# Performance work log

Measured on AMD Instinct MI355X. Metric: run time of the kernel, lower is better.

Reference implementation:

```python
import jax, jax.numpy as jnp
import numpy as np

N, E, D_IN, D_HID, D_OUT, G = 50000, 800000, 64, 64, 64, 64
BN_EPS = 1e-5


def gcn_conv(x, W, b, src, dst, n_nodes):
    """PyG GCNConv: add self-loops, sym-normalized sum aggregation, then bias.
    out_i = sum_{j->i} d_j^-1/2 d_i^-1/2 (x W)_j + d_i^-1 (x W)_i + b
    where d_i = 1 + in-degree(i) (self-loop included)."""
    h = x @ W  # [N, out]
    deg = jax.ops.segment_sum(jnp.ones((src.shape[0],), h.dtype), dst,
                              num_segments=n_nodes) + 1.0  # self-loop
    dinv = jax.lax.rsqrt(deg)  # deg >= 1 always
    coef = dinv[src] * dinv[dst]  # [E]
    msgs = h[src] * coef[:, None]  # [E, out] -- the big gather
    agg = jax.ops.segment_sum(msgs, dst, num_segments=n_nodes)
    agg = agg + h * (dinv * dinv)[:, None]  # self-loop messages
    return agg + b


def global_mean_pool(x, batch, n_graphs):
    sums = jax.ops.segment_sum(x, batch, num_segments=n_graphs)
    cnts = jax.ops.segment_sum(jnp.ones((x.shape[0],), x.dtype), batch,
                               num_segments=n_graphs)
    return sums / jnp.maximum(cnts, 1.0)[:, None]


def setup_inputs() -> dict:
    key = jax.random.key(0)
    ks = jax.random.split(key, 8)
    x = jax.random.normal(ks[0], (N, D_IN), dtype=jnp.float32)
    edge_index = jax.random.randint(ks[1], (2, E), 0, N, dtype=jnp.int32)
    batch = jnp.sort(jax.random.randint(ks[2], (N,), 0, G, dtype=jnp.int32))
    s1 = 1.0 / np.sqrt(D_IN)
    s2 = 1.0 / np.sqrt(D_HID)
    W1 = jax.random.uniform(ks[3], (D_IN, D_HID), jnp.float32, -s1, s1)
    b1 = jnp.zeros((D_HID,), jnp.float32)
    gamma = jnp.ones((D_HID,), jnp.float32)
    beta = jnp.zeros((D_HID,), jnp.float32)
    W2 = jax.random.uniform(ks[4], (D_HID, D_OUT), jnp.float32, -s2, s2)
    b2 = jnp.zeros((D_OUT,), jnp.float32)
    return {"x": x, "edge_index": edge_index, "batch": batch,
            "W1": W1, "b1": b1, "gamma": gamma, "beta": beta,
            "W2": W2, "b2": b2}


def reference(x, edge_index, batch, W1, b1, gamma, beta, W2, b2):
    src, dst = edge_index[0], edge_index[1]
    h = gcn_conv(x, W1, b1, src, dst, N)
    # BatchNorm1d with batch statistics (training-mode forward)
    mu = jnp.mean(h, axis=0)
    var = jnp.mean(jnp.square(h - mu), axis=0)
    h = (h - mu) * jax.lax.rsqrt(var + BN_EPS) * gamma + beta
    h = jax.nn.elu(h)
    # dropout is identity in eval / deterministic reference
    out = gcn_conv(h, W2, b2, src, dst, N)
    graph_rep = global_mean_pool(out, batch, G)
    return (out, graph_rep)
```

## Files before the change

kernel.cpp:

```cpp
#include <hip/hip_runtime.h>


constexpr int GGRAPHS = 64;
constexpr int EPB = 4096;
constexpr int CNTB = 128;
constexpr int ZBLK = 32;

__global__ void fat_phist_cnt_zero_mm64_kernel(
    const int* __restrict__ dst, const int* __restrict__ batch,
    int* __restrict__ hist, int* __restrict__ cntR, float* __restrict__ zbase,
    const float* __restrict__ X, const float* __restrict__ W,
    float* __restrict__ Y,
    int E, int n, int nblk, int nbuck) {
  __shared__ float Ws[64][64];
  __shared__ float xs[4][64];
  __shared__ int h[256];
  __shared__ int hb[GGRAPHS];
  int t = threadIdx.x;
  int bid = blockIdx.x;
  if (bid < nblk) {
    h[t] = 0;
    __syncthreads();
    int e0 = bid * EPB;
    int e1 = e0 + EPB < E ? e0 + EPB : E;
    for (int i = e0 + t; i < e1; i += 256) {
      int d = dst[i];
      if ((unsigned)d < (unsigned)n) atomicAdd(&h[d >> 8], 1);
    }
    __syncthreads();
    if (t < nbuck) hist[t * nblk + bid] = h[t];
  } else if (bid < nblk + CNTB) {
    int cb = bid - nblk;
    if (t < GGRAPHS) hb[t] = 0;
    __syncthreads();
    for (int i = cb * 256 + t; i < n; i += CNTB * 256) {
      int g = batch[i];
      if ((unsigned)g < (unsigned)GGRAPHS) atomicAdd(&hb[g], 1);
    }
    __syncthreads();
    if (t < GGRAPHS) cntR[cb * 64 + t] = hb[t];
  } else if (bid < nblk + CNTB + ZBLK) {
    int zb = bid - nblk - CNTB;
    float4 z4 = make_float4(0.f, 0.f, 0.f, 0.f);
    int tot4 = (256 * 128 + 16 * 4096) >> 2;
    float4* d4 = (float4*)zbase;
    for (int i = zb * 256 + t; i < tot4; i += ZBLK * 256) d4[i] = z4;
  } else {
    int mb = bid - nblk - CNTB - ZBLK;
    for (int i = t; i < 64 * 64; i += 256) Ws[i >> 6][i & 63] = W[i];
    int rr = t >> 6, c = t & 63;
    int row = mb * 4 + rr;
    xs[rr][c] = (row < n) ? X[(size_t)row * 64 + c] : 0.0f;
    __syncthreads();
    float acc = 0.0f;
#pragma unroll
    for (int k = 0; k < 64; ++k) acc = fmaf(xs[rr][k], Ws[k][c], acc);
    if (row < n) Y[(size_t)row * 64 + c] = acc;
  }
}

__global__ void scan1_kernel(const int* __restrict__ in, int* __restrict__ out,
                             int* __restrict__ bsum, int n) {
  __shared__ int tmp[256];
  int t = threadIdx.x;
  int i = blockIdx.x * 256 + t;
  int v = (i < n) ? in[i] : 0;
  tmp[t] = v;
  __syncthreads();
#pragma unroll
  for (int off = 1; off < 256; off <<= 1) {
    int a = (t >= off) ? tmp[t - off] : 0;
    __syncthreads();
    tmp[t] += a;
    __syncthreads();
  }
  if (i < n) out[i] = tmp[t] - v;
  if (t == 255) bsum[blockIdx.x] = tmp[255];
}

__global__ void part_kernel(const int* __restrict__ srcp, const int* __restrict__ dstp,
                            const int* __restrict__ hist, const int* __restrict__ bsum,
                            int* __restrict__ part, int E, int n, int nblk, int nbuck,
                            int nbt) {
  __shared__ int tmp[256];
  __shared__ int cur[256];
  int t = threadIdx.x;
  int v = (t < nbt) ? bsum[t] : 0;
  tmp[t] = v;
  __syncthreads();
#pragma unroll
  for (int off = 1; off < 256; off <<= 1) {
    int a = (t >= off) ? tmp[t - off] : 0;
    __syncthreads();
    tmp[t] += a;
    __syncthreads();
  }
  if (t < nbuck) {
    int idx = t * nblk + blockIdx.x;
    int tile = idx >> 8;
    int pre = (tile == 0) ? 0 : tmp[tile - 1];
    cur[t] = hist[idx] + pre;
  }
  __syncthreads();
  int e0 = blockIdx.x * EPB;
  int e1 = e0 + EPB < E ? e0 + EPB : E;
  for (int i = e0 + t; i < e1; i += 256) {
    int d = dstp[i];
    if ((unsigned)d >= (unsigned)n) continue;
    int s = srcp[i];
    int pos = atomicAdd(&cur[d >> 8], 1);
    part[pos] = (s << 8) | (d & 255);
  }
}

__global__ void csr_kernel(const int* __restrict__ part, const int* __restrict__ hist,
                           const int* __restrict__ bsum,
                           int* __restrict__ rowptr, float* __restrict__ dinv,
                           int* __restrict__ col, int n, int nblk, int nbuck,
                           int nbt, int S) {
  __shared__ int tmpb[256];
  __shared__ int degL[256], scn[256], cur[256];
  int t = threadIdx.x;
  int b = blockIdx.x;
  int v = (t < nbt) ? bsum[t] : 0;
  tmpb[t] = v;
  degL[t] = 0;
  cur[t] = 0;
  __syncthreads();
#pragma unroll
  for (int off = 1; off < 256; off <<= 1) {
    int a = (t >= off) ? tmpb[t - off] : 0;
    __syncthreads();
    tmpb[t] += a;
    __syncthreads();
  }
  int bidx = b * nblk;
  int eidx = bidx + nblk;
  int base = hist[bidx] + ((bidx >> 8) ? tmpb[(bidx >> 8) - 1] : 0);
  int total = tmpb[nbt - 1];
  int end = (eidx < S) ? hist[eidx] + ((eidx >> 8) ? tmpb[(eidx >> 8) - 1] : 0) : total;
  for (int i = base + t; i < end; i += 256) atomicAdd(&degL[part[i] & 255], 1);
  __syncthreads();
  int dv = degL[t];
  scn[t] = dv;
  __syncthreads();
#pragma unroll
  for (int off = 1; off < 256; off <<= 1) {
    int a = (t >= off) ? scn[t - off] : 0;
    __syncthreads();
    scn[t] += a;
    __syncthreads();
  }
  int excl = scn[t] - dv;
  int node = (b << 8) + t;
  if (node < n) {
    rowptr[node] = base + excl;
    dinv[node] = rsqrtf((float)dv + 1.0f);
  }
  if (b == nbuck - 1 && t == 0) rowptr[n] = end;
  scn[t] = excl;
  __syncthreads();
  for (int i = base + t; i < end; i += 256) {
    int u = part[i];
    int d = u & 255;
    int k = atomicAdd(&cur[d], 1);
    col[base + scn[d] + k] = u >> 8;
  }
}

__global__ void bn_elu_mm64_kernel(const float* __restrict__ X, const float* __restrict__ W,
                                   const float* __restrict__ ss, float* __restrict__ Y, int n) {
  __shared__ float Ws[64][64];
  __shared__ float xs[4][64];
  int tid = threadIdx.x;
  for (int i = tid; i < 64 * 64; i += 256) Ws[i >> 6][i & 63] = W[i];
  int rr = tid >> 6, c = tid & 63;
  int row = blockIdx.x * 4 + rr;
  float v = 0.0f;
  if (row < n) {
    v = X[(size_t)row * 64 + c] * ss[c] + ss[64 + c];
    v = v > 0.0f ? v : expm1f(v);
  }
  xs[rr][c] = v;
  __syncthreads();
  float acc = 0.0f;
#pragma unroll
  for (int k = 0; k < 64; ++k) acc = fmaf(xs[rr][k], Ws[k][c], acc);
  if (row < n) Y[(size_t)row * 64 + c] = acc;
}

__device__ __forceinline__ float4 gcn_gather_core(
    const int* __restrict__ rowptr, const int* __restrict__ col,
    const float* __restrict__ dinv, const float4* __restrict__ H4,
    int row, int lane, int sub, int cg, bool valid) {
  float4 acc = make_float4(0.f, 0.f, 0.f, 0.f);
  int p0 = 0, p1 = 0;
  if (valid) { p0 = rowptr[row]; p1 = rowptr[row + 1]; }
  for (int base = p0; base < p1; base += 64) {
    int myp = base + lane;
    int j = (myp < p1) ? col[myp] : 0;
    float w = (myp < p1) ? dinv[j] : 0.0f;
    int m = p1 - base;
    m = m < 64 ? m : 64;
#pragma unroll 4
    for (int k = 0; k < m; k += 4) {
      int s = k + sub;
      int jj = __shfl(j, s);
      float ww = __shfl(w, s);
      float4 hv = H4[(size_t)jj * 16 + cg];
      acc.x = fmaf(hv.x, ww, acc.x);
      acc.y = fmaf(hv.y, ww, acc.y);
      acc.z = fmaf(hv.z, ww, acc.z);
      acc.w = fmaf(hv.w, ww, acc.w);
    }
  }
  acc.x += __shfl_xor(acc.x, 16);
  acc.y += __shfl_xor(acc.y, 16);
  acc.z += __shfl_xor(acc.z, 16);
  acc.w += __shfl_xor(acc.w, 16);
  acc.x += __shfl_xor(acc.x, 32);
  acc.y += __shfl_xor(acc.y, 32);
  acc.z += __shfl_xor(acc.z, 32);
  acc.w += __shfl_xor(acc.w, 32);
  return acc;
}

__global__ void gather_bn_kernel(const int* __restrict__ rowptr, const int* __restrict__ col,
                                 const float* __restrict__ dinv, const float* __restrict__ H,
                                 const float* __restrict__ b, float* __restrict__ OUT,
                                 float* __restrict__ bnsR, int n) {
  int wave = threadIdx.x >> 6;
  int lane = threadIdx.x & 63;
  int row = blockIdx.x * 4 + wave;
  bool valid = row < n;
  int sub = lane >> 4;
  int cg = lane & 15;
  const float4* __restrict__ H4 = (const float4*)H;
  float4 acc = gcn_gather_core(rowptr, col, dinv, H4, row, lane, sub, cg, valid);
  float4 o = make_float4(0.f, 0.f, 0.f, 0.f);
  if (valid) {
    float di = dinv[row];
    float d2 = di * di;
    float4 self = H4[(size_t)row * 16 + cg];
    float4 bb = ((const float4*)b)[cg];
    o.x = fmaf(acc.x, di, fmaf(self.x, d2, bb.x));
    o.y = fmaf(acc.y, di, fmaf(self.y, d2, bb.y));
    o.z = fmaf(acc.z, di, fmaf(self.z, d2, bb.z));
    o.w = fmaf(acc.w, di, fmaf(self.w, d2, bb.w));
    if (sub == 0) ((float4*)OUT)[(size_t)row * 16 + cg] = o;
  }
  __shared__ float sA[4][64], sB[4][64];
  if (sub == 0) {
    sA[wave][4 * cg + 0] = o.x;
    sA[wave][4 * cg + 1] = o.y;
    sA[wave][4 * cg + 2] = o.z;
    sA[wave][4 * cg + 3] = o.w;
    sB[wave][4 * cg + 0] = o.x * o.x;
    sB[wave][4 * cg + 1] = o.y * o.y;
    sB[wave][4 * cg + 2] = o.z * o.z;
    sB[wave][4 * cg + 3] = o.w * o.w;
  }
  __syncthreads();
  int t = threadIdx.x;
  if (t < 64) {
    float s = sA[0][t] + sA[1][t] + sA[2][t] + sA[3][t];
    float s2 = sB[0][t] + sB[1][t] + sB[2][t] + sB[3][t];
    float* d = bnsR + (size_t)(blockIdx.x & 255) * 128;
    atomicAdd(&d[t], s);
    atomicAdd(&d[64 + t], s2);
  }
}

__global__ void gather_pool_kernel(const int* __restrict__ rowptr, const int* __restrict__ col,
                                   const float* __restrict__ dinv, const float* __restrict__ H,
                                   const float* __restrict__ b, float* __restrict__ OUT,
                                   const int* __restrict__ batch, float* __restrict__ poolR,
                                   int n) {
  int wave = threadIdx.x >> 6;
  int lane = threadIdx.x & 63;
  int row = blockIdx.x * 4 + wave;
  bool valid = row < n;
  int sub = lane >> 4;
  int cg = lane & 15;
  const float4* __restrict__ H4 = (const float4*)H;
  float4 acc = gcn_gather_core(rowptr, col, dinv, H4, row, lane, sub, cg, valid);
  float4 o = make_float4(0.f, 0.f, 0.f, 0.f);
  __shared__ float sO[4][64];
  __shared__ int sG[4];
  if (valid) {
    float di = dinv[row];
    float d2 = di * di;
    float4 self = H4[(size_t)row * 16 + cg];
    float4 bb = ((const float4*)b)[cg];
    o.x = fmaf(acc.x, di, fmaf(self.x, d2, bb.x));
    o.y = fmaf(acc.y, di, fmaf(self.y, d2, bb.y));
    o.z = fmaf(acc.z, di, fmaf(self.z, d2, bb.z));
    o.w = fmaf(acc.w, di, fmaf(self.w, d2, bb.w));
    if (sub == 0) ((float4*)OUT)[(size_t)row * 16 + cg] = o;
  }
  if (lane == 0) {
    int g = valid ? batch[row] : -1;
    sG[wave] = ((unsigned)g < (unsigned)GGRAPHS) ? g : -1;
  }
  if (sub == 0) {
    sO[wave][4 * cg + 0] = o.x;
    sO[wave][4 * cg + 1] = o.y;
    sO[wave][4 * cg + 2] = o.z;
    sO[wave][4 * cg + 3] = o.w;
  }
  __syncthreads();
  int t = threadIdx.x;
  if (t < 64) {
    float* base = poolR + (size_t)(blockIdx.x & 15) * 4096;
    int g0 = sG[0];
    float s0 = 0.0f;
#pragma unroll
    for (int w = 0; w < 4; ++w) {
      int gw = sG[w];
      if (gw < 0) continue;
      if (gw == g0) s0 += sO[w][t];
      else atomicAdd(&base[gw * 64 + t], sO[w][t]);
    }
    if (g0 >= 0) atomicAdd(&base[g0 * 64 + t], s0);
  }
}

__global__ void bn_final_kernel(const float* __restrict__ bnsR, const float* __restrict__ gamma,
                                const float* __restrict__ beta, float* __restrict__ ss, int n) {
  __shared__ float red[128];
  int t = threadIdx.x;
  float s = 0.0f;
  for (int r = 0; r < 256; ++r) s += bnsR[r * 128 + t];
  red[t] = s;
  __syncthreads();
  if (t < 64) {
    float inv_n = 1.0f / (float)n;
    float mu = red[t] * inv_n;
    float var = red[64 + t] * inv_n - mu * mu;
    var = fmaxf(var, 0.0f);
    float sc = gamma[t] * rsqrtf(var + 1e-5f);
    ss[t] = sc;
    ss[64 + t] = beta[t] - mu * sc;
  }
}

__global__ void pool_final_kernel(const float* __restrict__ poolR, const int* __restrict__ cntR,
                                  float* __restrict__ out) {
  __shared__ float cgc[64];
  int t = threadIdx.x;
  if (t < 64) {
    int g = (blockIdx.x * 256 + t) >> 6;
  }
  int idx = blockIdx.x * 256 + t;
  int g = idx >> 6;
  if (t < 4) {
    int gg = (blockIdx.x * 256) / 64 + t;
    int c = 0;
    for (int cb = 0; cb < CNTB; ++cb) c += cntR[cb * 64 + gg];
    cgc[t] = (float)c;
  }
  __syncthreads();
  float s = 0.0f;
  for (int r = 0; r < 16; ++r) s += poolR[r * 4096 + idx];
  out[idx] = s / fmaxf(cgc[(t >> 6)], 1.0f);
}

extern "C" void kernel_launch(void* const* d_in, const int* in_sizes, int n_in,
                              void* d_out, int out_size, void* d_ws, size_t ws_size,
                              hipStream_t stream) {
  const float* x = (const float*)d_in[0];
  const int* ei = (const int*)d_in[1];
  const int* batch = (const int*)d_in[2];
  const float* W1 = (const float*)d_in[3];
  const float* b1 = (const float*)d_in[4];
  const float* gamma = (const float*)d_in[5];
  const float* beta = (const float*)d_in[6];
  const float* W2 = (const float*)d_in[7];
  const float* b2 = (const float*)d_in[8];

  const int n = in_sizes[0] / 64;
  const int E = in_sizes[1] / 2;
  const int* srcp = ei;
  const int* dstp = ei + E;

  int nblkP = (E + EPB - 1) / EPB;
  int nbuck = (n + 255) >> 8;
  int S = nbuck * nblkP;
  int nbt = (S + 255) / 256;
  int gridRows = (n + 3) / 4;

  float* ws = (float*)d_ws;
  size_t nf = (size_t)n * 64;
  float* bufA = ws;
  float* bufB = ws + nf;
  float* dinv = ws + 2 * nf;
  float* ss = dinv + n;
  int* rowptr = (int*)(ss + 128);
  int* col = rowptr + n + 1;
  int* part = col + E;
  int* hist = part + E;
  int* bsum = hist + S + 1;
  float* bnsR = (float*)(((uintptr_t)(bsum + 256) + 15) & ~(uintptr_t)15);
  float* poolR = bnsR + 256 * 128;
  int* cntR = (int*)(poolR + 16 * 4096);

  float* out = (float*)d_out;

  int blk = 256;
  int fatGrid = nblkP + CNTB + ZBLK + gridRows;

  fat_phist_cnt_zero_mm64_kernel<<<fatGrid, blk, 0, stream>>>(
      dstp, batch, hist, cntR, bnsR, x, W1, bufA, E, n, nblkP, nbuck);
  scan1_kernel<<<nbt, blk, 0, stream>>>(hist, hist, bsum, S);
  part_kernel<<<nblkP, blk, 0, stream>>>(srcp, dstp, hist, bsum, part, E, n, nblkP,
                                         nbuck, nbt);
  csr_kernel<<<nbuck, blk, 0, stream>>>(part, hist, bsum, rowptr, dinv, col, n, nblkP,
                                        nbuck, nbt, S);

  gather_bn_kernel<<<gridRows, blk, 0, stream>>>(rowptr, col, dinv, bufA, b1, bufB, bnsR, n);
  bn_final_kernel<<<1, 128, 0, stream>>>(bnsR, gamma, beta, ss, n);
  bn_elu_mm64_kernel<<<gridRows, blk, 0, stream>>>(bufB, W2, ss, bufA, n);
  gather_pool_kernel<<<gridRows, blk, 0, stream>>>(rowptr, col, dinv, bufA, b2, out, batch,
                                                   poolR, n);
  pool_final_kernel<<<16, blk, 0, stream>>>(poolR, cntR, out + nf);
}
```

Measured before the change: 252.5 us.

## Spread X·W1 matmul blocks across the four CSR-build kernels to fill idle CUs

The first-layer 64x64 matmul, which previously ran entirely inside the first fat kernel, is split into four chunks. Each chunk is appended as extra blocks to one of the histogram, scan, partition and CSR kernels. The scan, partition and CSR stages launch few blocks, so this work fills otherwise idle compute units and shortens the serial chain. The split ratios are hand-tuned, and every kernel now reserves matmul shared memory, which may lower occupancy for the CSR blocks.

```diff
diff --git a/kernel.cpp b/kernel.cpp
--- a/kernel.cpp
+++ b/kernel.cpp
@@ -6,12 +6,26 @@
 constexpr int CNTB = 128;
 constexpr int ZBLK = 32;
 
-__global__ void fat_phist_cnt_zero_mm64_kernel(
+__device__ __forceinline__ void mm64_body(
+    const float* __restrict__ X, const float* __restrict__ W,
+    float* __restrict__ Y, float (*Ws)[64], float (*xs)[64],
+    int mb, int n, int t) {
+  for (int i = t; i < 64 * 64; i += 256) Ws[i >> 6][i & 63] = W[i];
+  int rr = t >> 6, c = t & 63;
+  int row = mb * 4 + rr;
+  xs[rr][c] = (row < n) ? X[(size_t)row * 64 + c] : 0.0f;
+  __syncthreads();
+  float acc = 0.0f;
+#pragma unroll
+  for (int k = 0; k < 64; ++k) acc = fmaf(xs[rr][k], Ws[k][c], acc);
+  if (row < n) Y[(size_t)row * 64 + c] = acc;
+}
+
+__global__ void fatA_kernel(
     const int* __restrict__ dst, const int* __restrict__ batch,
     int* __restrict__ hist, int* __restrict__ cntR, float* __restrict__ zbase,
     const float* __restrict__ X, const float* __restrict__ W,
-    float* __restrict__ Y,
-    int E, int n, int nblk, int nbuck) {
+    float* __restrict__ Y, int E, int n, int nblk, int nbuck, int c0) {
   __shared__ float Ws[64][64];
   __shared__ float xs[4][64];
   __shared__ int h[256];
@@ -46,125 +60,142 @@
     float4* d4 = (float4*)zbase;
     for (int i = zb * 256 + t; i < tot4; i += ZBLK * 256) d4[i] = z4;
   } else {
-    int mb = bid - nblk - CNTB - ZBLK;
-    for (int i = t; i < 64 * 64; i += 256) Ws[i >> 6][i & 63] = W[i];
-    int rr = t >> 6, c = t & 63;
-    int row = mb * 4 + rr;
-    xs[rr][c] = (row < n) ? X[(size_t)row * 64 + c] : 0.0f;
-    __syncthreads();
-    float acc = 0.0f;
-#pragma unroll
-    for (int k = 0; k < 64; ++k) acc = fmaf(xs[rr][k], Ws[k][c], acc);
-    if (row < n) Y[(size_t)row * 64 + c] = acc;
-  }
-}
-
-__global__ void scan1_kernel(const int* __restrict__ in, int* __restrict__ out,
-                             int* __restrict__ bsum, int n) {
+    mm64_body(X, W, Y, Ws, xs, c0 + (bid - nblk - CNTB - ZBLK), n, t);
+  }
+}
+
+__global__ void fatB_kernel(const int* __restrict__ in, int* __restrict__ outp,
+                            int* __restrict__ bsum,
+                            const float* __restrict__ X, const float* __restrict__ W,
+                            float* __restrict__ Y, int S, int n, int nbt, int c0) {
+  __shared__ float Ws[64][64];
+  __shared__ float xs[4][64];
   __shared__ int tmp[256];
   int t = threadIdx.x;
-  int i = blockIdx.x * 256 + t;
-  int v = (i < n) ? in[i] : 0;
-  tmp[t] = v;
-  __syncthreads();
-#pragma unroll
-  for (int off = 1; off < 256; off <<= 1) {
-    int a = (t >= off) ? tmp[t - off] : 0;
-    __syncthreads();
-    tmp[t] += a;
-    __syncthreads();
-  }
-  if (i < n) out[i] = tmp[t] - v;
-  if (t == 255) bsum[blockIdx.x] = tmp[255];
-}
-
-__global__ void part_kernel(const int* __restrict__ srcp, const int* __restrict__ dstp,
+  int bid = blockIdx.x;
+  if (bid < nbt) {
+    int i = bid * 256 + t;
+    int v = (i < S) ? in[i] : 0;
+    tmp[t] = v;
+    __syncthreads();
+#pragma unroll
+    for (int off = 1; off < 256; off <<= 1) {
+      int a = (t >= off) ? tmp[t - off] : 0;
+      __syncthreads();
+      tmp[t] += a;
+      __syncthreads();
+    }
+    if (i < S) outp[i] = tmp[t] - v;
+    if (t == 255) bsum[bid] = tmp[255];
+  } else {
+    mm64_body(X, W, Y, Ws, xs, c0 + (bid - nbt), n, t);
+  }
+}
+
+__global__ void fatC_kernel(const int* __restrict__ srcp, const int* __restrict__ dstp,
                             const int* __restrict__ hist, const int* __restrict__ bsum,
-                            int* __restrict__ part, int E, int n, int nblk, int nbuck,
-                            int nbt) {
+                            int* __restrict__ part,
+                            const float* __restrict__ X, const float* __restrict__ W,
+                            float* __restrict__ Y,
+                            int E, int n, int nblk, int nbuck, int nbt, int c0) {
+  __shared__ float Ws[64][64];
+  __shared__ float xs[4][64];
   __shared__ int tmp[256];
   __shared__ int cur[256];
   int t = threadIdx.x;
-  int v = (t < nbt) ? bsum[t] : 0;
-  tmp[t] = v;
-  __syncthreads();
-#pragma unroll
-  for (int off = 1; off < 256; off <<= 1) {
-    int a = (t >= off) ? tmp[t - off] : 0;
-    __syncthreads();
-    tmp[t] += a;
-    __syncthreads();
-  }
-  if (t < nbuck) {
-    int idx = t * nblk + blockIdx.x;
-    int tile = idx >> 8;
-    int pre = (tile == 0) ? 0 : tmp[tile - 1];
-    cur[t] = hist[idx] + pre;
-  }
-  __syncthreads();
-  int e0 = blockIdx.x * EPB;
-  int e1 = e0 + EPB < E ? e0 + EPB : E;
-  for (int i = e0 + t; i < e1; i += 256) {
-    int d = dstp[i];
-    if ((unsigned)d >= (unsigned)n) continue;
-    int s = srcp[i];
-    int pos = atomicAdd(&cur[d >> 8], 1);
-    part[pos] = (s << 8) | (d & 255);
-  }
-}
-
-__global__ void csr_kernel(const int* __restrict__ part, const int* __restrict__ hist,
-                           const int* __restrict__ bsum,
-                           int* __restrict__ rowptr, float* __restrict__ dinv,
-                           int* __restrict__ col, int n, int nblk, int nbuck,
-                           int nbt, int S) {
+  int bid = blockIdx.x;
+  if (bid < nblk) {
+    int v = (t < nbt) ? bsum[t] : 0;
+    tmp[t] = v;
+    __syncthreads();
+#pragma unroll
+    for (int off = 1; off < 256; off <<= 1) {
+      int a = (t >= off) ? tmp[t - off] : 0;
+      __syncthreads();
+      tmp[t] += a;
+      __syncthreads();
+    }
+    if (t < nbuck) {
+      int idx = t * nblk + bid;
+      int tile = idx >> 8;
+      int pre = (tile == 0) ? 0 : tmp[tile - 1];
+      cur[t] = hist[idx] + pre;
+    }
+    __syncthreads();
+    int e0 = bid * EPB;
+    int e1 = e0 + EPB < E ? e0 + EPB : E;
+    for (int i = e0 + t; i < e1; i += 256) {
+      int d = dstp[i];
+      if ((unsigned)d >= (unsigned)n) continue;
+      int s = srcp[i];
+      int pos = atomicAdd(&cur[d >> 8], 1);
+      part[pos] = (s << 8) | (d & 255);
+    }
+  } else {
+    mm64_body(X, W, Y, Ws, xs, c0 + (bid - nblk), n, t);
+  }
+}
+
+__global__ void fatD_kernel(const int* __restrict__ part, const int* __restrict__ hist,
+                            const int* __restrict__ bsum,
+                            int* __restrict__ rowptr, float* __restrict__ dinv,
+                            int* __restrict__ col,
+                            const float* __restrict__ X, const float* __restrict__ W,
+                            float* __restrict__ Y,
+                            int n, int nblk, int nbuck, int nbt, int S, int c0) {
+  __shared__ float Ws[64][64];
+  __shared__ float xs[4][64];
   __shared__ int tmpb[256];
   __shared__ int degL[256], scn[256], cur[256];
   int t = threadIdx.x;
   int b = blockIdx.x;
-  int v = (t < nbt) ? bsum[t] : 0;
-  tmpb[t] = v;
-  degL[t] = 0;
-  cur[t] = 0;
-  __syncthreads();
-#pragma unroll
-  for (int off = 1; off < 256; off <<= 1) {
-    int a = (t >= off) ? tmpb[t - off] : 0;
-    __syncthreads();
-    tmpb[t] += a;
-    __syncthreads();
-  }
-  int bidx = b * nblk;
-  int eidx = bidx + nblk;
-  int base = hist[bidx] + ((bidx >> 8) ? tmpb[(bidx >> 8) - 1] : 0);
-  int total = tmpb[nbt - 1];
-  int end = (eidx < S) ? hist[eidx] + ((eidx >> 8) ? tmpb[(eidx >> 8) - 1] : 0) : total;
-  for (int i = base + t; i < end; i += 256) atomicAdd(&degL[part[i] & 255], 1);
-  __syncthreads();
-  int dv = degL[t];
-  scn[t] = dv;
-  __syncthreads();
-#pragma unroll
-  for (int off = 1; off < 256; off <<= 1) {
-    int a = (t >= off) ? scn[t - off] : 0;
-    __syncthreads();
-    scn[t] += a;
-    __syncthreads();
-  }
-  int excl = scn[t] - dv;
-  int node = (b << 8) + t;
-  if (node < n) {
-    rowptr[node] = base + excl;
-    dinv[node] = rsqrtf((float)dv + 1.0f);
-  }
-  if (b == nbuck - 1 && t == 0) rowptr[n] = end;
-  scn[t] = excl;
-  __syncthreads();
-  for (int i = base + t; i < end; i += 256) {
-    int u = part[i];
-    int d = u & 255;
-    int k = atomicAdd(&cur[d], 1);
-    col[base + scn[d] + k] = u >> 8;
+  if (b < nbuck) {
+    int v = (t < nbt) ? bsum[t] : 0;
+    tmpb[t] = v;
+    degL[t] = 0;
+    cur[t] = 0;
+    __syncthreads();
+#pragma unroll
+    for (int off = 1; off < 256; off <<= 1) {
+      int a = (t >= off) ? tmpb[t - off] : 0;
+      __syncthreads();
+      tmpb[t] += a;
+      __syncthreads();
+    }
+    int bidx = b * nblk;
+    int eidx = bidx + nblk;
+    int base = hist[bidx] + ((bidx >> 8) ? tmpb[(bidx >> 8) - 1] : 0);
+    int total = tmpb[nbt - 1];
+    int end = (eidx < S) ? hist[eidx] + ((eidx >> 8) ? tmpb[(eidx >> 8) - 1] : 0) : total;
+    for (int i = base + t; i < end; i += 256) atomicAdd(&degL[part[i] & 255], 1);
+    __syncthreads();
+    int dv = degL[t];
+    scn[t] = dv;
+    __syncthreads();
+#pragma unroll
+    for (int off = 1; off < 256; off <<= 1) {
+      int a = (t >= off) ? scn[t - off] : 0;
+      __syncthreads();
+      scn[t] += a;
+      __syncthreads();
+    }
+    int excl = scn[t] - dv;
+    int node = (b << 8) + t;
+    if (node < n) {
+      rowptr[node] = base + excl;
+      dinv[node] = rsqrtf((float)dv + 1.0f);
+    }
+    if (b == nbuck - 1 && t == 0) rowptr[n] = end;
+    scn[t] = excl;
+    __syncthreads();
+    for (int i = base + t; i < end; i += 256) {
+      int u = part[i];
+      int d = u & 255;
+      int k = atomicAdd(&cur[d], 1);
+      col[base + scn[d] + k] = u >> 8;
+    }
+  } else {
+    mm64_body(X, W, Y, Ws, xs, c0 + (b - nbuck), n, t);
   }
 }
 
@@ -348,11 +379,7 @@
                                   float* __restrict__ out) {
   __shared__ float cgc[64];
   int t = threadIdx.x;
-  if (t < 64) {
-    int g = (blockIdx.x * 256 + t) >> 6;
-  }
   int idx = blockIdx.x * 256 + t;
-  int g = idx >> 6;
   if (t < 4) {
     int gg = (blockIdx.x * 256) / 64 + t;
     int c = 0;
@@ -388,6 +415,11 @@
   int S = nbuck * nblkP;
   int nbt = (S + 255) / 256;
   int gridRows = (n + 3) / 4;
+
+  int C1 = gridRows * 28 / 100;
+  int C2 = gridRows * 12 / 100;
+  int C3 = gridRows * 26 / 100;
+  int C4 = gridRows - C1 - C2 - C3;
 
   float* ws = (float*)d_ws;
   size_t nf = (size_t)n * 64;
@@ -407,15 +439,15 @@
   float* out = (float*)d_out;
 
   int blk = 256;
-  int fatGrid = nblkP + CNTB + ZBLK + gridRows;
-
-  fat_phist_cnt_zero_mm64_kernel<<<fatGrid, blk, 0, stream>>>(
-      dstp, batch, hist, cntR, bnsR, x, W1, bufA, E, n, nblkP, nbuck);
-  scan1_kernel<<<nbt, blk, 0, stream>>>(hist, hist, bsum, S);
-  part_kernel<<<nblkP, blk, 0, stream>>>(srcp, dstp, hist, bsum, part, E, n, nblkP,
-                                         nbuck, nbt);
-  csr_kernel<<<nbuck, blk, 0, stream>>>(part, hist, bsum, rowptr, dinv, col, n, nblkP,
-                                        nbuck, nbt, S);
+
+  fatA_kernel<<<nblkP + CNTB + ZBLK + C1, blk, 0, stream>>>(
+      dstp, batch, hist, cntR, bnsR, x, W1, bufA, E, n, nblkP, nbuck, 0);
+  fatB_kernel<<<nbt + C2, blk, 0, stream>>>(hist, hist, bsum, x, W1, bufA, S, n, nbt, C1);
+  fatC_kernel<<<nblkP + C3, blk, 0, stream>>>(srcp, dstp, hist, bsum, part, x, W1, bufA,
+                                              E, n, nblkP, nbuck, nbt, C1 + C2);
+  fatD_kernel<<<nbuck + C4, blk, 0, stream>>>(part, hist, bsum, rowptr, dinv, col,
+                                              x, W1, bufA, n, nblkP, nbuck, nbt, S,
+                                              C1 + C2 + C3);
 
   gather_bn_kernel<<<gridRows, blk, 0, stream>>>(rowptr, col, dinv, bufA, b1, bufB, bnsR, n);
   bn_final_kernel<<<1, 128, 0, stream>>>(bnsR, gamma, beta, ss, n);
```

Measured after the change: 240.7 us. 1.05x faster.
